# Kernel optimization log

Measured on AMD Instinct MI355X. Metric: run time of the kernel, lower is better.

## Reference

```python
import jax, jax.numpy as jnp
import numpy as np

B, L1, L2 = 4, 512, 512
K1D, K2D, V1D, V2D, A = 256, 256, 256, 256, 128


def setup_inputs() -> dict:
    key = jax.random.key(0)
    ks = jax.random.split(key, 12)
    n = lambda i, shape, sc=1.0: (jax.random.normal(ks[i], shape, jnp.float32) * sc)
    return {
        "k1": n(0, (B, L1, K1D)),
        "k2": n(1, (B, L2, K2D)),
        "v1": n(2, (B, L1, V1D)),
        "v2": n(3, (B, L2, V2D)),
        "W1": n(4, (K1D, A), 0.05),
        "b1": n(5, (A,), 0.05),
        "W2": n(6, (K2D, A), 0.05),
        "b2": n(7, (A,), 0.05),
        "ws": n(8, (A,), 0.05),
        "bs": n(9, (), 0.05),
        # lengths in [L/2, L) so every softmax row has at least one finite entry
        "k1_lengths": jax.random.randint(ks[10], (B,), L1 // 2, L1, dtype=jnp.int32),
        "k2_lengths": jax.random.randint(ks[11], (B,), L2 // 2, L2, dtype=jnp.int32),
    }


def reference(k1, k2, v1, v2, W1, b1, W2, b2, ws, bs, k1_lengths, k2_lengths):
    # projected keys: [B,L1,A], [B,L2,A]
    p1 = jnp.einsum("bik,ka->bia", k1, W1) + b1
    p2 = jnp.einsum("bjk,ka->bja", k2, W2) + b2
    h = jnp.tanh(p1[:, :, None, :] + p2[:, None, :, :])  # [B,L1,L2,A]
    score = jnp.einsum("bija,a->bij", h, ws) + bs
    # torch mask semantics: +1 for padded k1 rows, +1 for padded k2 cols, mask where sum == 1
    row_pad = (jnp.arange(L1)[None, :] >= k1_lengths[:, None]).astype(jnp.int32)  # [B,L1]
    col_pad = (jnp.arange(L2)[None, :] >= k2_lengths[:, None]).astype(jnp.int32)  # [B,L2]
    mask = (row_pad[:, :, None] + col_pad[:, None, :]) == 1  # [B,L1,L2]
    score = jnp.where(mask, -jnp.inf, score)
    w1 = jax.nn.softmax(jnp.transpose(score, (0, 2, 1)), axis=-1)  # [B,L2,L1], softmax over L1
    w2 = jax.nn.softmax(score, axis=-1)                             # [B,L1,L2], softmax over L2
    o1 = jnp.matmul(w1, v1)  # [B,L2,V1D]
    o2 = jnp.matmul(w2, v2)  # [B,L1,V2D]
    return (o1, o2, w1, w2, score)
```

## Files before the change

kernel.cpp:

```cpp
#include <hip/hip_runtime.h>
#include <math.h>

#define NB 4
#define NL1 512
#define NL2 512
#define NKD 256
#define NA 128
#define NV 256

#define O1_OFF 0
#define O2_OFF (NB*NL2*NV)
#define W1_OFF (O2_OFF + NB*NL1*NV)
#define W2_OFF (W1_OFF + NB*NL2*NL1)
#define SC_OFF (W2_OFF + NB*NL1*NL2)

#define MASK_NEG (-1e30f)

#define SC2LOG2E 2.8853900817779268f

#if __has_builtin(__builtin_amdgcn_exp2f)
#define EXP2F(x) __builtin_amdgcn_exp2f(x)
#else
#define EXP2F(x) __expf((x) * 0.6931471805599453f)
#endif
#if __has_builtin(__builtin_amdgcn_rcpf)
#define RCPF(x) __builtin_amdgcn_rcpf(x)
#else
#define RCPF(x) (1.0f / (x))
#endif

__device__ __forceinline__ unsigned short f2bf(float f) {
    unsigned u = __float_as_uint(f);
    u += 0x7fffu + ((u >> 16) & 1u);
    return (unsigned short)(u >> 16);
}
__device__ __forceinline__ unsigned pk2bf(float a, float b) {
    return (unsigned)f2bf(a) | ((unsigned)f2bf(b) << 16);
}

__global__ __launch_bounds__(128) void proj_kernel(
    const float* __restrict__ k1, const float* __restrict__ k2,
    const float* __restrict__ W1, const float* __restrict__ b1,
    const float* __restrict__ W2, const float* __restrict__ b2,
    const float* __restrict__ v1, const float* __restrict__ v2,
    float* __restrict__ p1, float* __restrict__ p2,
    unsigned* __restrict__ v1t, unsigned* __restrict__ v2t)
{
    __shared__ float kr[4][NKD];
    __shared__ float trbuf[32][68];
    int blk = blockIdx.x;
    int tid = threadIdx.x;
    if (blk >= 1024) {
        int idx = blk - 1024;
        int t = idx >> 8;
        int rem = idx & 255;
        int b = rem >> 6;
        int rem2 = rem & 63;
        int d0 = (rem2 >> 4) * 64;
        int s0 = (rem2 & 15) * 32;
        const float* Vsrc = (t ? v2 : v1) + (size_t)b * NL2 * NV;
        unsigned* Vdst    = (t ? v2t : v1t) + (size_t)b * NV * (NL2/2);
        #pragma unroll
        for (int u = 0; u < 4; u++) {
            int i2 = tid + 128 * u;
            int r = i2 >> 4, c = i2 & 15;
            *(float4*)&trbuf[r][c*4] = *(const float4*)&Vsrc[(size_t)(s0 + r) * NV + d0 + c*4];
        }
        __syncthreads();
        #pragma unroll
        for (int u = 0; u < 8; u++) {
            int i2 = tid + 128 * u;
            int dd = i2 >> 4, c = i2 & 15;
            Vdst[(size_t)(d0 + dd) * (NL2/2) + (s0 >> 1) + c] =
                pk2bf(trbuf[2*c][dd], trbuf[2*c+1][dd]);
        }
        return;
    }
    const float *K, *W, *bias; float* P; int rowbase;
    if (blk < (NB*NL1)/4) { K = k1; W = W1; bias = b1; P = p1; rowbase = blk*4; }
    else                  { K = k2; W = W2; bias = b2; P = p2; rowbase = (blk - (NB*NL1)/4)*4; }
    for (int idx = tid; idx < 256; idx += 128) {
        int r = idx >> 6, c = idx & 63;
        *(float4*)&kr[r][c*4] = *(const float4*)&K[(rowbase + r)*NKD + c*4];
    }
    __syncthreads();
    int a = tid;
    float acc0 = bias[a], acc1 = bias[a], acc2 = bias[a], acc3 = bias[a];
    #pragma unroll 4
    for (int k = 0; k < NKD; k++) {
        float wv = W[k*NA + a];
        acc0 = fmaf(kr[0][k], wv, acc0);
        acc1 = fmaf(kr[1][k], wv, acc1);
        acc2 = fmaf(kr[2][k], wv, acc2);
        acc3 = fmaf(kr[3][k], wv, acc3);
    }
    float s0 = fminf(fmaxf(acc0 * SC2LOG2E, -50.f), 50.f);
    float s1 = fminf(fmaxf(acc1 * SC2LOG2E, -50.f), 50.f);
    float s2 = fminf(fmaxf(acc2 * SC2LOG2E, -50.f), 50.f);
    float s3 = fminf(fmaxf(acc3 * SC2LOG2E, -50.f), 50.f);
    P[(rowbase+0)*NA + a] = EXP2F(s0);
    P[(rowbase+1)*NA + a] = EXP2F(s1);
    P[(rowbase+2)*NA + a] = EXP2F(s2);
    P[(rowbase+3)*NA + a] = EXP2F(s3);
}

#define P1_STRIDE 132
#define P2_STRIDE 68

__global__ __launch_bounds__(256) void score_kernel(
    const float* __restrict__ p1, const float* __restrict__ p2,
    const float* __restrict__ ws, const float* __restrict__ bs,
    const int* __restrict__ len1, const int* __restrict__ len2,
    float* __restrict__ score, float* __restrict__ w1pre)
{
    __shared__ float p1t[64][P1_STRIDE];
    __shared__ float p2t[NA][P2_STRIDE];
    __shared__ float wst[NA];
    __shared__ float wsum[2];
    int b  = blockIdx.z;
    int i0 = blockIdx.y * 64, j0 = blockIdx.x * 64;
    int tid = threadIdx.x;
    if (tid < 128) {
        float w = ws[tid];
        wst[tid] = -2.0f * w;
        float v = w;
        #pragma unroll
        for (int o = 32; o > 0; o >>= 1) v += __shfl_xor(v, o);
        if ((tid & 63) == 0) wsum[tid >> 6] = v;
    }
    const float* p1src = p1 + (b*NL1 + i0)*NA;
    const float* p2src = p2 + (b*NL2 + j0)*NA;
    for (int idx = tid; idx < 2048; idx += 256) {
        int r = idx >> 5, c = idx & 31;
        *(float4*)&p1t[r][c*4] = *(const float4*)&p1src[r*NA + c*4];
    }
    for (int idx = tid; idx < 2048; idx += 256) {
        int j = idx >> 5, c = idx & 31;
        float4 t = *(const float4*)&p2src[j*NA + c*4];
        p2t[c*4+0][j] = t.x; p2t[c*4+1][j] = t.y;
        p2t[c*4+2][j] = t.z; p2t[c*4+3][j] = t.w;
    }
    __syncthreads();

    int tx = tid & 15, ty = tid >> 4;
    int il = ty*4, jl = tx*4;
    float acc[4][4] = {};
    #pragma unroll 2
    for (int a = 0; a < NA; a += 4) {
        float4 wv = *(float4*)&wst[a];
        float4 x0 = *(float4*)&p1t[il  ][a];
        float4 x1 = *(float4*)&p1t[il+1][a];
        float4 x2 = *(float4*)&p1t[il+2][a];
        float4 x3 = *(float4*)&p1t[il+3][a];
        float4 y0 = *(float4*)&p2t[a  ][jl];
        float4 y1 = *(float4*)&p2t[a+1][jl];
        float4 y2 = *(float4*)&p2t[a+2][jl];
        float4 y3 = *(float4*)&p2t[a+3][jl];
        #define TRM(r,c,xq,yq,wq) acc[r][c] = fmaf(wq, RCPF(fmaf(xq, yq, 1.0f)), acc[r][c])
        #define QROW(q, yv, wq) \
            TRM(0,0, x0.q, yv.x, wq); TRM(0,1, x0.q, yv.y, wq); TRM(0,2, x0.q, yv.z, wq); TRM(0,3, x0.q, yv.w, wq); \
            TRM(1,0, x1.q, yv.x, wq); TRM(1,1, x1.q, yv.y, wq); TRM(1,2, x1.q, yv.z, wq); TRM(1,3, x1.q, yv.w, wq); \
            TRM(2,0, x2.q, yv.x, wq); TRM(2,1, x2.q, yv.y, wq); TRM(2,2, x2.q, yv.z, wq); TRM(2,3, x2.q, yv.w, wq); \
            TRM(3,0, x3.q, yv.x, wq); TRM(3,1, x3.q, yv.y, wq); TRM(3,2, x3.q, yv.z, wq); TRM(3,3, x3.q, yv.w, wq)
        QROW(x, y0, wv.x);
        QROW(y, y1, wv.y);
        QROW(z, y2, wv.z);
        QROW(w, y3, wv.w);
        #undef QROW
        #undef TRM
    }
    float sb = wsum[0] + wsum[1] + bs[0];
    int n1 = len1[b], n2 = len2[b];
    float mv[4][4];
    #pragma unroll
    for (int di = 0; di < 4; di++) {
        int gi = i0 + il + di;
        int rp = (gi >= n1);
        #pragma unroll
        for (int dj = 0; dj < 4; dj++) {
            int gj = j0 + jl + dj;
            float val = acc[di][dj] + sb;
            int cp = (gj >= n2);
            if (rp + cp == 1) val = MASK_NEG;
            mv[di][dj] = val;
        }
    }
    #pragma unroll
    for (int di = 0; di < 4; di++) {
        float4 v = make_float4(mv[di][0], mv[di][1], mv[di][2], mv[di][3]);
        *(float4*)&score[(size_t)(b*NL1 + i0 + il + di)*NL2 + j0 + jl] = v;
    }
    #pragma unroll
    for (int dj = 0; dj < 4; dj++) {
        float4 v = make_float4(mv[0][dj], mv[1][dj], mv[2][dj], mv[3][dj]);
        *(float4*)&w1pre[((size_t)b*NL2 + j0 + jl + dj)*NL1 + i0 + il] = v;
    }
}

__global__ __launch_bounds__(256) void softmax_both(const float* __restrict__ score,
                                                    float* __restrict__ w2,
                                                    float* __restrict__ w1,
                                                    unsigned* __restrict__ w2bf,
                                                    unsigned* __restrict__ w1bf)
{
    int row = blockIdx.x * 4 + (threadIdx.x >> 6);
    int lane = threadIdx.x & 63;
    const float* s; float* d; unsigned* dbf;
    if (row < NB*NL1) {
        s = score + (size_t)row * NL2; d = w2 + (size_t)row * NL2;
        dbf = w2bf + (size_t)row * (NL2/2);
    } else {
        size_t r = row - NB*NL1;
        s = w1 + r * NL1; d = w1 + r * NL1;
        dbf = w1bf + r * (NL1/2);
    }
    float4 v0 = *(const float4*)&s[lane * 4];
    float4 v1 = *(const float4*)&s[256 + lane * 4];
    float m = fmaxf(fmaxf(fmaxf(v0.x, v0.y), fmaxf(v0.z, v0.w)),
                    fmaxf(fmaxf(v1.x, v1.y), fmaxf(v1.z, v1.w)));
    #pragma unroll
    for (int o = 32; o > 0; o >>= 1) m = fmaxf(m, __shfl_xor(m, o));
    float4 e0, e1;
    e0.x = __expf(v0.x - m); e0.y = __expf(v0.y - m);
    e0.z = __expf(v0.z - m); e0.w = __expf(v0.w - m);
    e1.x = __expf(v1.x - m); e1.y = __expf(v1.y - m);
    e1.z = __expf(v1.z - m); e1.w = __expf(v1.w - m);
    float sum = (e0.x + e0.y) + (e0.z + e0.w) + (e1.x + e1.y) + (e1.z + e1.w);
    #pragma unroll
    for (int o = 32; o > 0; o >>= 1) sum += __shfl_xor(sum, o);
    float inv = 1.0f / sum;
    e0.x *= inv; e0.y *= inv; e0.z *= inv; e0.w *= inv;
    e1.x *= inv; e1.y *= inv; e1.z *= inv; e1.w *= inv;
    *(float4*)&d[lane * 4] = e0;
    *(float4*)&d[256 + lane * 4] = e1;
    uint2 lo = make_uint2(pk2bf(e0.x, e0.y), pk2bf(e0.z, e0.w));
    uint2 hi = make_uint2(pk2bf(e1.x, e1.y), pk2bf(e1.z, e1.w));
    *(uint2*)&dbf[lane * 2] = lo;
    *(uint2*)&dbf[128 + lane * 2] = hi;
}

typedef __attribute__((ext_vector_type(8))) short bf16x8;
typedef __attribute__((ext_vector_type(4))) float f32x4;

#define KT 264

__global__ __launch_bounds__(512) void out_matmul(
    const unsigned* __restrict__ w2bf, const unsigned* __restrict__ w1bf,
    const unsigned* __restrict__ v2t,  const unsigned* __restrict__ v1t,
    float* __restrict__ o2, float* __restrict__ o1)
{
    __shared__ unsigned short Wt[64 * KT];
    __shared__ unsigned short Vt[64 * KT];
    int z = blockIdx.z; int b = z >> 1, m = z & 1;
    const unsigned* Wb = (m ? w1bf : w2bf) + (size_t)b * NL1 * (NL2/2);
    const unsigned* Vb = (m ? v1t : v2t)   + (size_t)b * NV * (NL2/2);
    float*          Om = (m ? o1 : o2)     + (size_t)b * NL1 * NV;
    int r0 = blockIdx.y * 64, d0 = blockIdx.x * 64;
    int tid = threadIdx.x;
    int lane = tid & 63, wid = tid >> 6;
    int ry = wid & 3, cx = wid >> 2;
    int lm = lane & 15, kg = lane >> 4;

    const unsigned short* Wf  = &Wt[(ry * 16 + lm) * KT];
    const unsigned short* Vlo = &Vt[(cx * 32 + lm) * KT];
    const unsigned short* Vhi = Vlo + 16 * KT;

    f32x4 acc0 = {0.f,0.f,0.f,0.f}, acc1 = {0.f,0.f,0.f,0.f};

    int wr = tid >> 3, c0 = tid & 7;
    for (int h = 0; h < 2; h++) {
        if (h) __syncthreads();
        const unsigned* srcW = Wb + (size_t)(r0 + wr) * (NL2/2) + h * 128;
        const unsigned* srcV = Vb + (size_t)(d0 + wr) * (NL2/2) + h * 128;
        unsigned short* dstW = &Wt[wr * KT];
        unsigned short* dstV = &Vt[wr * KT];
        #pragma unroll
        for (int k = 0; k < 4; k++) {
            int c = c0 + 8 * k;
            *(uint4*)&dstW[c * 8] = *(const uint4*)&srcW[c * 4];
            *(uint4*)&dstV[c * 8] = *(const uint4*)&srcV[c * 4];
        }
        __syncthreads();
        #pragma unroll 4
        for (int t = 0; t < 8; t++) {
            int s0 = t * 32 + 8 * kg;
            bf16x8 fa  = *(const bf16x8*)(Wf  + s0);
            bf16x8 fb0 = *(const bf16x8*)(Vlo + s0);
            bf16x8 fb1 = *(const bf16x8*)(Vhi + s0);
            acc0 = __builtin_amdgcn_mfma_f32_16x16x32_bf16(fa, fb0, acc0, 0, 0, 0);
            acc1 = __builtin_amdgcn_mfma_f32_16x16x32_bf16(fa, fb1, acc1, 0, 0, 0);
        }
    }

    int rlo = r0 + ry * 16 + 4 * kg;
    int clo = d0 + cx * 32 + lm;
    #pragma unroll
    for (int e = 0; e < 4; e++) {
        Om[(size_t)(rlo + e) * NV + clo]      = acc0[e];
        Om[(size_t)(rlo + e) * NV + clo + 16] = acc1[e];
    }
}

extern "C" void kernel_launch(void* const* d_in, const int* in_sizes, int n_in,
                              void* d_out, int out_size, void* d_ws, size_t ws_size,
                              hipStream_t stream) {
    const float* k1  = (const float*)d_in[0];
    const float* k2  = (const float*)d_in[1];
    const float* v1  = (const float*)d_in[2];
    const float* v2  = (const float*)d_in[3];
    const float* W1  = (const float*)d_in[4];
    const float* b1  = (const float*)d_in[5];
    const float* W2  = (const float*)d_in[6];
    const float* b2  = (const float*)d_in[7];
    const float* wsv = (const float*)d_in[8];
    const float* bsp = (const float*)d_in[9];
    const int* len1  = (const int*)d_in[10];
    const int* len2  = (const int*)d_in[11];

    float* out   = (float*)d_out;
    float* o1    = out + O1_OFF;
    float* o2    = out + O2_OFF;
    float* w1    = out + W1_OFF;
    float* w2    = out + W2_OFF;
    float* score = out + SC_OFF;

    float* p1       = (float*)d_ws;
    float* p2       = p1 + NB*NL1*NA;
    unsigned* w2bf  = (unsigned*)(p2 + NB*NL2*NA);
    unsigned* w1bf  = w2bf + (size_t)NB*NL1*(NL2/2);
    unsigned* v2t   = w1bf + (size_t)NB*NL2*(NL1/2);
    unsigned* v1t   = v2t + (size_t)NB*NV*(NL2/2);

    proj_kernel<<<dim3((NB*NL1)/4 + (NB*NL2)/4 + 512), 128, 0, stream>>>(
        k1, k2, W1, b1, W2, b2, v1, v2, p1, p2, v1t, v2t);
    score_kernel<<<dim3(NL2/64, NL1/64, NB), 256, 0, stream>>>(p1, p2, wsv, bsp, len1, len2, score, w1);
    softmax_both<<<dim3((NB*NL1 + NB*NL2)/4), 256, 0, stream>>>(score, w2, w1, w2bf, w1bf);
    out_matmul<<<dim3(NV/64, NL1/64, NB*2), 512, 0, stream>>>(w2bf, w1bf, v2t, v1t, o2, o1);
}
```

Before: 60.25 us.

## Fuse row softmax into output matmul, drop separate softmax kernel and bf16 buffers

Removes the standalone softmax kernel. The output matmul block now loads its 64 full score rows (fp32), computes max/sum/normalise across 8 threads per row, packs bf16 straight into LDS, and the blocks with d0==0 write the fp32 softmax weights out. The V tile is loaded once with full K, so the two-phase loop and its extra sync go away. The aim is to save a launch and the global round-trip of the bf16 weight copies. In exchange, each of the four column blocks recomputes the softmax for the same rows, and the larger LDS footprint (KT=520) may reduce occupancy.

```diff
diff --git a/kernel.cpp b/kernel.cpp
--- a/kernel.cpp
+++ b/kernel.cpp
@@ -197,99 +197,91 @@
     }
 }
 
-__global__ __launch_bounds__(256) void softmax_both(const float* __restrict__ score,
-                                                    float* __restrict__ w2,
-                                                    float* __restrict__ w1,
-                                                    unsigned* __restrict__ w2bf,
-                                                    unsigned* __restrict__ w1bf)
-{
-    int row = blockIdx.x * 4 + (threadIdx.x >> 6);
-    int lane = threadIdx.x & 63;
-    const float* s; float* d; unsigned* dbf;
-    if (row < NB*NL1) {
-        s = score + (size_t)row * NL2; d = w2 + (size_t)row * NL2;
-        dbf = w2bf + (size_t)row * (NL2/2);
-    } else {
-        size_t r = row - NB*NL1;
-        s = w1 + r * NL1; d = w1 + r * NL1;
-        dbf = w1bf + r * (NL1/2);
-    }
-    float4 v0 = *(const float4*)&s[lane * 4];
-    float4 v1 = *(const float4*)&s[256 + lane * 4];
-    float m = fmaxf(fmaxf(fmaxf(v0.x, v0.y), fmaxf(v0.z, v0.w)),
-                    fmaxf(fmaxf(v1.x, v1.y), fmaxf(v1.z, v1.w)));
-    #pragma unroll
-    for (int o = 32; o > 0; o >>= 1) m = fmaxf(m, __shfl_xor(m, o));
-    float4 e0, e1;
-    e0.x = __expf(v0.x - m); e0.y = __expf(v0.y - m);
-    e0.z = __expf(v0.z - m); e0.w = __expf(v0.w - m);
-    e1.x = __expf(v1.x - m); e1.y = __expf(v1.y - m);
-    e1.z = __expf(v1.z - m); e1.w = __expf(v1.w - m);
-    float sum = (e0.x + e0.y) + (e0.z + e0.w) + (e1.x + e1.y) + (e1.z + e1.w);
-    #pragma unroll
-    for (int o = 32; o > 0; o >>= 1) sum += __shfl_xor(sum, o);
-    float inv = 1.0f / sum;
-    e0.x *= inv; e0.y *= inv; e0.z *= inv; e0.w *= inv;
-    e1.x *= inv; e1.y *= inv; e1.z *= inv; e1.w *= inv;
-    *(float4*)&d[lane * 4] = e0;
-    *(float4*)&d[256 + lane * 4] = e1;
-    uint2 lo = make_uint2(pk2bf(e0.x, e0.y), pk2bf(e0.z, e0.w));
-    uint2 hi = make_uint2(pk2bf(e1.x, e1.y), pk2bf(e1.z, e1.w));
-    *(uint2*)&dbf[lane * 2] = lo;
-    *(uint2*)&dbf[128 + lane * 2] = hi;
-}
-
 typedef __attribute__((ext_vector_type(8))) short bf16x8;
 typedef __attribute__((ext_vector_type(4))) float f32x4;
 
-#define KT 264
+#define KT 520
 
 __global__ __launch_bounds__(512) void out_matmul(
-    const unsigned* __restrict__ w2bf, const unsigned* __restrict__ w1bf,
-    const unsigned* __restrict__ v2t,  const unsigned* __restrict__ v1t,
-    float* __restrict__ o2, float* __restrict__ o1)
+    const float* __restrict__ scoreSrc, const float* __restrict__ w1preSrc,
+    const unsigned* __restrict__ v2t,   const unsigned* __restrict__ v1t,
+    float* __restrict__ o2, float* __restrict__ o1,
+    float* __restrict__ w2out, float* __restrict__ w1out)
 {
     __shared__ unsigned short Wt[64 * KT];
     __shared__ unsigned short Vt[64 * KT];
     int z = blockIdx.z; int b = z >> 1, m = z & 1;
-    const unsigned* Wb = (m ? w1bf : w2bf) + (size_t)b * NL1 * (NL2/2);
-    const unsigned* Vb = (m ? v1t : v2t)   + (size_t)b * NV * (NL2/2);
-    float*          Om = (m ? o1 : o2)     + (size_t)b * NL1 * NV;
+    const float*    Sm = (m ? w1preSrc : scoreSrc) + (size_t)b * NL1 * NL2;
+    const unsigned* Vb = (m ? v1t : v2t) + (size_t)b * NV * (NL2/2);
+    float* Om   = (m ? o1 : o2)       + (size_t)b * NL1 * NV;
+    float* Wout = (m ? w1out : w2out) + (size_t)b * NL1 * NL2;
     int r0 = blockIdx.y * 64, d0 = blockIdx.x * 64;
     int tid = threadIdx.x;
     int lane = tid & 63, wid = tid >> 6;
     int ry = wid & 3, cx = wid >> 2;
     int lm = lane & 15, kg = lane >> 4;
+    int wr = tid >> 3, c0 = tid & 7;
+
+    {
+        const unsigned* srcV = Vb + (size_t)(d0 + wr) * (NL2/2);
+        unsigned short* dstV = &Vt[wr * KT];
+        #pragma unroll
+        for (int k = 0; k < 8; k++) {
+            int c = c0 + 8 * k;
+            *(uint4*)&dstV[c * 8] = *(const uint4*)&srcV[c * 4];
+        }
+    }
+    {
+        const float* srcR = Sm + (size_t)(r0 + wr) * 512;
+        float4 f[16];
+        #pragma unroll
+        for (int k = 0; k < 16; k++) f[k] = *(const float4*)&srcR[(c0 + 8*k) * 4];
+        float mx = -3.4e38f;
+        #pragma unroll
+        for (int k = 0; k < 16; k++)
+            mx = fmaxf(mx, fmaxf(fmaxf(f[k].x, f[k].y), fmaxf(f[k].z, f[k].w)));
+        #pragma unroll
+        for (int o = 1; o <= 4; o <<= 1) mx = fmaxf(mx, __shfl_xor(mx, o));
+        float sum = 0.f;
+        #pragma unroll
+        for (int k = 0; k < 16; k++) {
+            f[k].x = __expf(f[k].x - mx); f[k].y = __expf(f[k].y - mx);
+            f[k].z = __expf(f[k].z - mx); f[k].w = __expf(f[k].w - mx);
+            sum += (f[k].x + f[k].y) + (f[k].z + f[k].w);
+        }
+        #pragma unroll
+        for (int o = 1; o <= 4; o <<= 1) sum += __shfl_xor(sum, o);
+        float inv = 1.0f / sum;
+        unsigned* dstW = (unsigned*)&Wt[wr * KT];
+        #pragma unroll
+        for (int k = 0; k < 16; k++) {
+            f[k].x *= inv; f[k].y *= inv; f[k].z *= inv; f[k].w *= inv;
+            int c = c0 + 8 * k;
+            uint2 p = make_uint2(pk2bf(f[k].x, f[k].y), pk2bf(f[k].z, f[k].w));
+            *(uint2*)&dstW[c * 2] = p;
+        }
+        if (d0 == 0) {
+            float* orow = Wout + (size_t)(r0 + wr) * 512;
+            #pragma unroll
+            for (int k = 0; k < 16; k++)
+                *(float4*)&orow[(c0 + 8*k) * 4] = f[k];
+        }
+    }
+    __syncthreads();
 
     const unsigned short* Wf  = &Wt[(ry * 16 + lm) * KT];
     const unsigned short* Vlo = &Vt[(cx * 32 + lm) * KT];
     const unsigned short* Vhi = Vlo + 16 * KT;
 
     f32x4 acc0 = {0.f,0.f,0.f,0.f}, acc1 = {0.f,0.f,0.f,0.f};
-
-    int wr = tid >> 3, c0 = tid & 7;
-    for (int h = 0; h < 2; h++) {
-        if (h) __syncthreads();
-        const unsigned* srcW = Wb + (size_t)(r0 + wr) * (NL2/2) + h * 128;
-        const unsigned* srcV = Vb + (size_t)(d0 + wr) * (NL2/2) + h * 128;
-        unsigned short* dstW = &Wt[wr * KT];
-        unsigned short* dstV = &Vt[wr * KT];
-        #pragma unroll
-        for (int k = 0; k < 4; k++) {
-            int c = c0 + 8 * k;
-            *(uint4*)&dstW[c * 8] = *(const uint4*)&srcW[c * 4];
-            *(uint4*)&dstV[c * 8] = *(const uint4*)&srcV[c * 4];
-        }
-        __syncthreads();
-        #pragma unroll 4
-        for (int t = 0; t < 8; t++) {
-            int s0 = t * 32 + 8 * kg;
-            bf16x8 fa  = *(const bf16x8*)(Wf  + s0);
-            bf16x8 fb0 = *(const bf16x8*)(Vlo + s0);
-            bf16x8 fb1 = *(const bf16x8*)(Vhi + s0);
-            acc0 = __builtin_amdgcn_mfma_f32_16x16x32_bf16(fa, fb0, acc0, 0, 0, 0);
-            acc1 = __builtin_amdgcn_mfma_f32_16x16x32_bf16(fa, fb1, acc1, 0, 0, 0);
-        }
+    #pragma unroll 4
+    for (int t = 0; t < 16; t++) {
+        int s0 = t * 32 + 8 * kg;
+        bf16x8 fa  = *(const bf16x8*)(Wf  + s0);
+        bf16x8 fb0 = *(const bf16x8*)(Vlo + s0);
+        bf16x8 fb1 = *(const bf16x8*)(Vhi + s0);
+        acc0 = __builtin_amdgcn_mfma_f32_16x16x32_bf16(fa, fb0, acc0, 0, 0, 0);
+        acc1 = __builtin_amdgcn_mfma_f32_16x16x32_bf16(fa, fb1, acc1, 0, 0, 0);
     }
 
     int rlo = r0 + ry * 16 + 4 * kg;
@@ -326,14 +318,12 @@
 
     float* p1       = (float*)d_ws;
     float* p2       = p1 + NB*NL1*NA;
-    unsigned* w2bf  = (unsigned*)(p2 + NB*NL2*NA);
-    unsigned* w1bf  = w2bf + (size_t)NB*NL1*(NL2/2);
-    unsigned* v2t   = w1bf + (size_t)NB*NL2*(NL1/2);
+    float* w1pre    = p2 + NB*NL2*NA;
+    unsigned* v2t   = (unsigned*)(w1pre + (size_t)NB*NL2*NL1);
     unsigned* v1t   = v2t + (size_t)NB*NV*(NL2/2);
 
     proj_kernel<<<dim3((NB*NL1)/4 + (NB*NL2)/4 + 512), 128, 0, stream>>>(
         k1, k2, W1, b1, W2, b2, v1, v2, p1, p2, v1t, v2t);
-    score_kernel<<<dim3(NL2/64, NL1/64, NB), 256, 0, stream>>>(p1, p2, wsv, bsp, len1, len2, score, w1);
-    softmax_both<<<dim3((NB*NL1 + NB*NL2)/4), 256, 0, stream>>>(score, w2, w1, w2bf, w1bf);
-    out_matmul<<<dim3(NV/64, NL1/64, NB*2), 512, 0, stream>>>(w2bf, w1bf, v2t, v1t, o2, o1);
-}
+    score_kernel<<<dim3(NL2/64, NL1/64, NB), 256, 0, stream>>>(p1, p2, wsv, bsp, len1, len2, score, w1pre);
+    out_matmul<<<dim3(NV/64, NL1/64, NB*2), 512, 0, stream>>>(score, w1pre, v2t, v1t, o2, o1, w2, w1);
+}
```

Result: slower. 61.58 us (+2.2%).
